# Kernel optimization log

Measured on AMD Instinct MI355X. Metric: run time of the kernel, lower is better.

The kernel has to match this reference:

```python
import jax, jax.numpy as jnp
import numpy as np

B, IN, H, U = 65536, 128, 256, 256

def lecun_tanh(x):
    return 1.7159 * jnp.tanh(0.666 * x)

def _xavier(key, shape):
    fan_out, fan_in = shape
    limit = np.sqrt(6.0 / (fan_in + fan_out))
    return jax.random.uniform(key, shape, jnp.float32, -limit, limit)

def setup_inputs() -> dict:
    key = jax.random.key(0)
    ks = jax.random.split(key, 12)
    return {
        "input": jax.random.normal(ks[0], (B, IN), jnp.float32),
        "hx": jax.random.normal(ks[1], (B, H), jnp.float32),
        "ts": jax.random.uniform(ks[2], (B, 1), jnp.float32),
        # backbone Linear(IN+H -> U)
        "Wb": _xavier(ks[3], (U, IN + H)),
        "bb": jnp.zeros((U,), jnp.float32),
        # ff1, ff2, time_a, time_b: Linear(U -> H)
        "W1": _xavier(ks[4], (H, U)),
        "b1": jnp.zeros((H,), jnp.float32),
        "W2": _xavier(ks[5], (H, U)),
        "b2": jnp.zeros((H,), jnp.float32),
        "Wa": _xavier(ks[6], (H, U)),
        "ba": jnp.zeros((H,), jnp.float32),
        "Wt": _xavier(ks[7], (H, U)),
        "bt": jnp.zeros((H,), jnp.float32),
    }

def reference(input, hx, ts, Wb, bb, W1, b1, W2, b2, Wa, ba, Wt, bt):
    # x = cat([input, hx]) -> backbone MLP (1 layer, LeCun tanh)
    x = jnp.concatenate([input, hx], axis=1)          # [B, IN+H]
    x = lecun_tanh(x @ Wb.T + bb)                     # [B, U]
    ff1 = jnp.tanh(x @ W1.T + b1)                     # [B, H]
    ff2 = jnp.tanh(x @ W2.T + b2)
    t_a = x @ Wa.T + ba
    t_b = x @ Wt.T + bt
    t_interp = jax.nn.sigmoid(t_a * ts + t_b)         # ts broadcasts [B,1]
    new_hidden = ff1 * (1.0 - t_interp) + t_interp * ff2
    return new_hidden
```

## Files before the change

kernel.cpp:

```cpp
#include <hip/hip_runtime.h>

typedef float v4f __attribute__((ext_vector_type(4)));
typedef short v8s __attribute__((ext_vector_type(8)));

#define BM 64

__device__ __forceinline__ unsigned short f2bf(float f) {
    union { float f; unsigned u; } v; v.f = f;
    unsigned u = v.u;
    u += 0x7FFFu + ((u >> 16) & 1u);
    return (unsigned short)(u >> 16);
}

__device__ __forceinline__ unsigned cvt_pk_bf16(float lo, float hi) {
    unsigned r;
    asm("v_cvt_pk_bf16_f32 %0, %1, %2" : "=v"(r) : "v"(lo), "v"(hi));
    return r;
}

#define LDS_BARRIER() do {                                        \
    asm volatile("s_waitcnt lgkmcnt(0)" ::: "memory");            \
    __builtin_amdgcn_s_barrier();                                 \
    __builtin_amdgcn_sched_barrier(0);                            \
} while (0)

#define SB() __builtin_amdgcn_sched_barrier(0)

__device__ __forceinline__ float fast_exp2(float x) {
#if __has_builtin(__builtin_amdgcn_exp2f)
    return __builtin_amdgcn_exp2f(x);
#else
    return exp2f(x);
#endif
}
__device__ __forceinline__ float fast_rcp(float x) {
#if __has_builtin(__builtin_amdgcn_rcpf)
    return __builtin_amdgcn_rcpf(x);
#else
    return 1.0f / x;
#endif
}
__device__ __forceinline__ float fast_tanh(float y) {
    float t = fast_exp2(y * 2.885390081777927f);
    return (t - 1.0f) * fast_rcp(t + 1.0f);
}
__device__ __forceinline__ float fast_sigmoid(float z) {
    float t = fast_exp2(-1.4426950408889634f * z);
    return fast_rcp(1.0f + t);
}

__global__ void prep_pack(const float* __restrict__ Wb, const float* __restrict__ W1,
                          const float* __restrict__ W2, const float* __restrict__ Wa,
                          const float* __restrict__ Wt, unsigned short* __restrict__ ws)
{
    int e = blockIdx.x * 256 + threadIdx.x;
    if (e >= 360448) return;
    const float* src; int K; int base;
    if (e < 98304)       { src = Wb; K = 384; base = 0; }
    else if (e < 163840) { src = W1; K = 256; base = 98304; }
    else if (e < 229376) { src = W2; K = 256; base = 163840; }
    else if (e < 294912) { src = Wa; K = 256; base = 229376; }
    else                 { src = Wt; K = 256; base = 294912; }
    int le   = e - base;
    int j    = le & 7;
    int lane = (le >> 3) & 63;
    int tile = le >> 9;
    int kt   = K >> 5;
    int ks   = tile % kt;
    int nt   = tile / kt;
    int n = nt * 16 + (lane & 15);
    int k = ks * 32 + (lane >> 4) * 8 + j;
    ws[e] = f2bf(src[n * K + k]);
}

__global__ __launch_bounds__(256, 2) void cfc_fused(
    const float* __restrict__ xin, const float* __restrict__ hx,
    const float* __restrict__ ts,
    const float* __restrict__ bb, const float* __restrict__ b1,
    const float* __restrict__ b2, const float* __restrict__ ba,
    const float* __restrict__ bt,
    const unsigned short* __restrict__ wpk,
    float* __restrict__ out)
{
    __shared__ unsigned short lds[16384];
    const int tid  = threadIdx.x;
    const int lane = tid & 63;
    const int w    = tid >> 6;
    const int row0 = blockIdx.x * BM;

    v8s br0[4], br1[4], br2[4];

#define BLOAD(S, DST) do {                                                    \
    _Pragma("unroll")                                                         \
    for (int i = 0; i < 4; ++i) {                                             \
        size_t goff;                                                          \
        if ((S) < 12) {                                                       \
            goff = (size_t)((w * 4 + i) * 12 + (S)) * 512;                    \
        } else {                                                              \
            int s2_ = (S) - 12, g_ = s2_ >> 3, ks_ = s2_ & 7;                 \
            goff = 98304u + (size_t)i * 65536                                 \
                 + (size_t)((w * 4 + g_) * 8 + ks_) * 512;                    \
        }                                                                     \
        DST[i] = *reinterpret_cast<const v8s*>(wpk + goff + (size_t)lane * 8);\
    }                                                                         \
} while (0)

#define ISSUE_IN(SRC, LD, BUF) do {                                           \
    _Pragma("unroll")                                                         \
    for (int it = 0; it < 4; ++it) {                                          \
        int i_ = tid + it * 256; int r_ = i_ >> 4; int c4_ = i_ & 15;         \
        BUF[it] = *(reinterpret_cast<const v4f*>((SRC) + (size_t)r_ * (LD)) + c4_); \
    }                                                                         \
} while (0)

#define WRITE_IN(BUF) do {                                                    \
    _Pragma("unroll")                                                         \
    for (int it = 0; it < 4; ++it) {                                          \
        int i_ = tid + it * 256; int r_ = i_ >> 4; int c4_ = i_ & 15;         \
        uint2 pk_;                                                            \
        pk_.x = cvt_pk_bf16(BUF[it][0], BUF[it][1]);                          \
        pk_.y = cvt_pk_bf16(BUF[it][2], BUF[it][3]);                          \
        int idx_ = (((r_ >> 4) * 2 + (c4_ >> 3)) * 64 + ((c4_ >> 1) & 3) * 16 \
                    + (r_ & 15)) * 8 + (c4_ & 1) * 4;                         \
        *reinterpret_cast<uint2*>(&lds[idx_]) = pk_;                          \
    }                                                                         \
} while (0)

#define P1STEP(S, CUR, PRE) do {                                              \
    BLOAD((S) + 2, PRE);                                                      \
    v8s aa_[4];                                                               \
    _Pragma("unroll")                                                         \
    for (int mt = 0; mt < 4; ++mt)                                            \
        aa_[mt] = *reinterpret_cast<const v8s*>(                              \
                      &lds[((mt * 2 + ((S) & 1)) * 64 + lane) * 8]);          \
    __builtin_amdgcn_s_setprio(1);                                            \
    _Pragma("unroll")                                                         \
    for (int nt = 0; nt < 4; ++nt)                                            \
        _Pragma("unroll")                                                     \
        for (int mt = 0; mt < 4; ++mt)                                        \
            acc[nt][mt] = __builtin_amdgcn_mfma_f32_16x16x32_bf16(            \
                              aa_[mt], CUR[nt], acc[nt][mt], 0, 0, 0);        \
    __builtin_amdgcn_s_setprio(0);                                            \
    SB();                                                                     \
} while (0)

#define P2STEP(S, KS, CUR, PRE) do {                                          \
    BLOAD((S) + 2, PRE);                                                      \
    v8s aa_[4];                                                               \
    _Pragma("unroll")                                                         \
    for (int mt = 0; mt < 4; ++mt)                                            \
        aa_[mt] = *reinterpret_cast<const v8s*>(                              \
                      &lds[((mt * 8 + (KS)) * 64 + lane) * 8]);               \
    __builtin_amdgcn_s_setprio(1);                                            \
    _Pragma("unroll")                                                         \
    for (int mat = 0; mat < 4; ++mat)                                         \
        _Pragma("unroll")                                                     \
        for (int mt = 0; mt < 4; ++mt)                                        \
            a2[mat][mt] = __builtin_amdgcn_mfma_f32_16x16x32_bf16(            \
                              aa_[mt], CUR[mat], a2[mat][mt], 0, 0, 0);       \
    __builtin_amdgcn_s_setprio(0);                                            \
    SB();                                                                     \
} while (0)

#define P2STEP_NS(S, KS, CUR) do {                                            \
    v8s aa_[4];                                                               \
    _Pragma("unroll")                                                         \
    for (int mt = 0; mt < 4; ++mt)                                            \
        aa_[mt] = *reinterpret_cast<const v8s*>(                              \
                      &lds[((mt * 8 + (KS)) * 64 + lane) * 8]);               \
    __builtin_amdgcn_s_setprio(1);                                            \
    _Pragma("unroll")                                                         \
    for (int mat = 0; mat < 4; ++mat)                                         \
        _Pragma("unroll")                                                     \
        for (int mt = 0; mt < 4; ++mt)                                        \
            a2[mat][mt] = __builtin_amdgcn_mfma_f32_16x16x32_bf16(            \
                              aa_[mt], CUR[mat], a2[mat][mt], 0, 0, 0);       \
    __builtin_amdgcn_s_setprio(0);                                            \
    SB();                                                                     \
} while (0)

#define GINIT(G) do {                                                         \
    const int n_ = w * 64 + (G) * 16 + (lane & 15);                           \
    float v1_ = b1[n_], v2_ = b2[n_], va_ = ba[n_], vt_ = bt[n_];             \
    v4f q1_ = {v1_,v1_,v1_,v1_}, q2_ = {v2_,v2_,v2_,v2_};                     \
    v4f qa_ = {va_,va_,va_,va_}, qt_ = {vt_,vt_,vt_,vt_};                     \
    _Pragma("unroll")                                                         \
    for (int mt = 0; mt < 4; ++mt) {                                          \
        a2[0][mt] = q1_; a2[1][mt] = q2_; a2[2][mt] = qa_; a2[3][mt] = qt_;   \
    }                                                                         \
} while (0)

#define EPI(G) do {                                                           \
    const int n_ = w * 64 + (G) * 16 + (lane & 15);                           \
    _Pragma("unroll")                                                         \
    for (int mt = 0; mt < 4; ++mt) {                                          \
        int rowb_ = row0 + mt * 16 + ((lane >> 4) << 2);                      \
        v4f tsv_ = *reinterpret_cast<const v4f*>(&ts[rowb_]);                 \
        _Pragma("unroll")                                                     \
        for (int r = 0; r < 4; ++r) {                                         \
            float ff1_ = fast_tanh(a2[0][mt][r]);                             \
            float ff2_ = fast_tanh(a2[1][mt][r]);                             \
            float ti_  = fast_sigmoid(a2[2][mt][r] * tsv_[r] + a2[3][mt][r]); \
            out[(size_t)(rowb_ + r) * 256 + n_] = ff1_ + ti_ * (ff2_ - ff1_); \
        }                                                                     \
    }                                                                         \
} while (0)

    v4f acc[4][4];
    #pragma unroll
    for (int nt = 0; nt < 4; ++nt) {
        float bv = bb[w * 64 + nt * 16 + (lane & 15)];
        v4f bvv = {bv, bv, bv, bv};
        #pragma unroll
        for (int mt = 0; mt < 4; ++mt) acc[nt][mt] = bvv;
    }

    v4f sA[4], sB[4];
    ISSUE_IN(xin + (size_t)row0 * 128, 128, sA);
    BLOAD(0, br0); BLOAD(1, br1);
    WRITE_IN(sA);
    ISSUE_IN(xin + (size_t)row0 * 128 + 64, 128, sB);
    LDS_BARRIER();
    P1STEP(0, br0, br2); P1STEP(1, br1, br0);
    LDS_BARRIER();
    WRITE_IN(sB);
    ISSUE_IN(hx + (size_t)row0 * 256, 256, sA);
    LDS_BARRIER();
    P1STEP(2, br2, br1); P1STEP(3, br0, br2);
    LDS_BARRIER();
    WRITE_IN(sA);
    ISSUE_IN(hx + (size_t)row0 * 256 + 64, 256, sB);
    LDS_BARRIER();
    P1STEP(4, br1, br0); P1STEP(5, br2, br1);
    LDS_BARRIER();
    WRITE_IN(sB);
    ISSUE_IN(hx + (size_t)row0 * 256 + 128, 256, sA);
    LDS_BARRIER();
    P1STEP(6, br0, br2); P1STEP(7, br1, br0);
    LDS_BARRIER();
    WRITE_IN(sA);
    ISSUE_IN(hx + (size_t)row0 * 256 + 192, 256, sB);
    LDS_BARRIER();
    P1STEP(8, br2, br1); P1STEP(9, br0, br2);
    LDS_BARRIER();
    WRITE_IN(sB);
    LDS_BARRIER();
    P1STEP(10, br1, br0); P1STEP(11, br2, br1);

    LDS_BARRIER();

    #pragma unroll
    for (int nt = 0; nt < 4; ++nt)
        #pragma unroll
        for (int mt = 0; mt < 4; ++mt)
            #pragma unroll
            for (int r = 0; r < 4; ++r) {
                float xv = 1.7159f * fast_tanh(0.666f * acc[nt][mt][r]);
                int idx = ((mt*8 + w*2 + (nt >> 1)) * 64
                           + ((nt & 1)*2 + ((lane >> 3) & 1)) * 16 + (lane >> 4)*4 + r) * 8
                          + (lane & 7);
                lds[idx] = f2bf(xv);
            }
    LDS_BARRIER();

    v4f a2[4][4];
    GINIT(0);
    P2STEP(12,0, br0, br2); P2STEP(13,1, br1, br0);
    P2STEP(14,2, br2, br1); P2STEP(15,3, br0, br2);
    P2STEP(16,4, br1, br0); P2STEP(17,5, br2, br1);
    P2STEP(18,6, br0, br2); P2STEP(19,7, br1, br0);
    EPI(0);
    GINIT(1);
    P2STEP(20,0, br2, br1); P2STEP(21,1, br0, br2);
    P2STEP(22,2, br1, br0); P2STEP(23,3, br2, br1);
    P2STEP(24,4, br0, br2); P2STEP(25,5, br1, br0);
    P2STEP(26,6, br2, br1); P2STEP(27,7, br0, br2);
    EPI(1);
    GINIT(2);
    P2STEP(28,0, br1, br0); P2STEP(29,1, br2, br1);
    P2STEP(30,2, br0, br2); P2STEP(31,3, br1, br0);
    P2STEP(32,4, br2, br1); P2STEP(33,5, br0, br2);
    P2STEP(34,6, br1, br0); P2STEP(35,7, br2, br1);
    EPI(2);
    GINIT(3);
    P2STEP(36,0, br0, br2); P2STEP(37,1, br1, br0);
    P2STEP(38,2, br2, br1); P2STEP(39,3, br0, br2);
    P2STEP(40,4, br1, br0); P2STEP(41,5, br2, br1);
    P2STEP_NS(42,6, br0);   P2STEP_NS(43,7, br1);
    EPI(3);

#undef BLOAD
#undef ISSUE_IN
#undef WRITE_IN
#undef P1STEP
#undef P2STEP
#undef P2STEP_NS
#undef GINIT
#undef EPI
}

extern "C" void kernel_launch(void* const* d_in, const int* in_sizes, int n_in,
                              void* d_out, int out_size, void* d_ws, size_t ws_size,
                              hipStream_t stream)
{
    const float* xin = (const float*)d_in[0];
    const float* hx  = (const float*)d_in[1];
    const float* ts  = (const float*)d_in[2];
    const float* Wb  = (const float*)d_in[3];
    const float* bb  = (const float*)d_in[4];
    const float* W1  = (const float*)d_in[5];
    const float* b1  = (const float*)d_in[6];
    const float* W2  = (const float*)d_in[7];
    const float* b2  = (const float*)d_in[8];
    const float* Wa  = (const float*)d_in[9];
    const float* ba  = (const float*)d_in[10];
    const float* Wt  = (const float*)d_in[11];
    const float* bt  = (const float*)d_in[12];

    if (ws_size < 360448 * sizeof(unsigned short)) return;
    unsigned short* wpk = (unsigned short*)d_ws;

    prep_pack<<<1408, 256, 0, stream>>>(Wb, W1, W2, Wa, Wt, wpk);
    cfc_fused<<<1024, 256, 0, stream>>>(xin, hx, ts, bb, b1, b2, ba, bt, wpk,
                                        (float*)d_out);
}
```

Baseline: 68.40 us.

## Split fused CfC kernel into backbone and head kernels via bf16 workspace

Splits the single fused kernel into two launches when the workspace is large enough. The first computes the backbone layer and writes the activated x as bf16 in MFMA fragment layout to global memory. The second reads those fragments straight from global memory (no LDS) to run the four head GEMMs and the epilogue, and uses higher occupancy (launch bounds 3). It also collapses the fused kernel's double input staging buffer into one. The aim is to relieve register and LDS pressure in each phase, at the cost of an extra 32 MB round trip through global memory and one more launch.

```diff
diff --git a/kernel.cpp b/kernel.cpp
--- a/kernel.cpp
+++ b/kernel.cpp
@@ -73,6 +73,243 @@
     ws[e] = f2bf(src[n * K + k]);
 }
 
+__global__ __launch_bounds__(256, 2) void cfc_p1(
+    const float* __restrict__ xin, const float* __restrict__ hx,
+    const float* __restrict__ bb, const unsigned short* __restrict__ wpk,
+    unsigned short* __restrict__ Xg)
+{
+    __shared__ unsigned short lds[16384];
+    const int tid  = threadIdx.x;
+    const int lane = tid & 63;
+    const int w    = tid >> 6;
+    const int row0 = blockIdx.x * BM;
+
+    v8s br0[4], br1[4], br2[4];
+
+#define BLOADA(S, DST) do {                                                   \
+    _Pragma("unroll")                                                         \
+    for (int i = 0; i < 4; ++i) {                                             \
+        size_t goff = (size_t)((w * 4 + i) * 12 + ((S) % 12)) * 512;          \
+        DST[i] = *reinterpret_cast<const v8s*>(wpk + goff + (size_t)lane * 8);\
+    }                                                                         \
+} while (0)
+
+#define ISSUE_INA(SRC, LD, BUF) do {                                          \
+    _Pragma("unroll")                                                         \
+    for (int it = 0; it < 4; ++it) {                                          \
+        int i_ = tid + it * 256; int r_ = i_ >> 4; int c4_ = i_ & 15;         \
+        BUF[it] = *(reinterpret_cast<const v4f*>((SRC) + (size_t)r_ * (LD)) + c4_); \
+    }                                                                         \
+} while (0)
+
+#define WRITE_INA(BUF) do {                                                   \
+    _Pragma("unroll")                                                         \
+    for (int it = 0; it < 4; ++it) {                                          \
+        int i_ = tid + it * 256; int r_ = i_ >> 4; int c4_ = i_ & 15;         \
+        uint2 pk_;                                                            \
+        pk_.x = cvt_pk_bf16(BUF[it][0], BUF[it][1]);                          \
+        pk_.y = cvt_pk_bf16(BUF[it][2], BUF[it][3]);                          \
+        int idx_ = (((r_ >> 4) * 2 + (c4_ >> 3)) * 64 + ((c4_ >> 1) & 3) * 16 \
+                    + (r_ & 15)) * 8 + (c4_ & 1) * 4;                         \
+        *reinterpret_cast<uint2*>(&lds[idx_]) = pk_;                          \
+    }                                                                         \
+} while (0)
+
+#define P1STEPA(S, CUR, PRE) do {                                             \
+    BLOADA((S) + 2, PRE);                                                     \
+    v8s aa_[4];                                                               \
+    _Pragma("unroll")                                                         \
+    for (int mt = 0; mt < 4; ++mt)                                            \
+        aa_[mt] = *reinterpret_cast<const v8s*>(                              \
+                      &lds[((mt * 2 + ((S) & 1)) * 64 + lane) * 8]);          \
+    __builtin_amdgcn_s_setprio(1);                                            \
+    _Pragma("unroll")                                                         \
+    for (int nt = 0; nt < 4; ++nt)                                            \
+        _Pragma("unroll")                                                     \
+        for (int mt = 0; mt < 4; ++mt)                                        \
+            acc[nt][mt] = __builtin_amdgcn_mfma_f32_16x16x32_bf16(            \
+                              aa_[mt], CUR[nt], acc[nt][mt], 0, 0, 0);        \
+    __builtin_amdgcn_s_setprio(0);                                            \
+    SB();                                                                     \
+} while (0)
+
+    v4f acc[4][4];
+    #pragma unroll
+    for (int nt = 0; nt < 4; ++nt) {
+        float bv = bb[w * 64 + nt * 16 + (lane & 15)];
+        v4f bvv = {bv, bv, bv, bv};
+        #pragma unroll
+        for (int mt = 0; mt < 4; ++mt) acc[nt][mt] = bvv;
+    }
+
+    v4f sA[4];
+    ISSUE_INA(xin + (size_t)row0 * 128, 128, sA);
+    BLOADA(0, br0); BLOADA(1, br1);
+    WRITE_INA(sA);
+    ISSUE_INA(xin + (size_t)row0 * 128 + 64, 128, sA);
+    LDS_BARRIER();
+    P1STEPA(0, br0, br2); P1STEPA(1, br1, br0);
+    LDS_BARRIER();
+    WRITE_INA(sA);
+    ISSUE_INA(hx + (size_t)row0 * 256, 256, sA);
+    LDS_BARRIER();
+    P1STEPA(2, br2, br1); P1STEPA(3, br0, br2);
+    LDS_BARRIER();
+    WRITE_INA(sA);
+    ISSUE_INA(hx + (size_t)row0 * 256 + 64, 256, sA);
+    LDS_BARRIER();
+    P1STEPA(4, br1, br0); P1STEPA(5, br2, br1);
+    LDS_BARRIER();
+    WRITE_INA(sA);
+    ISSUE_INA(hx + (size_t)row0 * 256 + 128, 256, sA);
+    LDS_BARRIER();
+    P1STEPA(6, br0, br2); P1STEPA(7, br1, br0);
+    LDS_BARRIER();
+    WRITE_INA(sA);
+    ISSUE_INA(hx + (size_t)row0 * 256 + 192, 256, sA);
+    LDS_BARRIER();
+    P1STEPA(8, br2, br1); P1STEPA(9, br0, br2);
+    LDS_BARRIER();
+    WRITE_INA(sA);
+    LDS_BARRIER();
+    P1STEPA(10, br1, br0); P1STEPA(11, br2, br1);
+
+    LDS_BARRIER();
+
+    #pragma unroll
+    for (int nt = 0; nt < 4; ++nt)
+        #pragma unroll
+        for (int mt = 0; mt < 4; ++mt)
+            #pragma unroll
+            for (int r = 0; r < 4; ++r) {
+                float xv = 1.7159f * fast_tanh(0.666f * acc[nt][mt][r]);
+                int idx = ((mt*8 + w*2 + (nt >> 1)) * 64
+                           + ((nt & 1)*2 + ((lane >> 3) & 1)) * 16 + (lane >> 4)*4 + r) * 8
+                          + (lane & 7);
+                lds[idx] = f2bf(xv);
+            }
+    LDS_BARRIER();
+
+    unsigned short* xb = Xg + (size_t)blockIdx.x * 16384;
+    #pragma unroll
+    for (int it = 0; it < 8; ++it) {
+        int i = tid + it * 256;
+        *reinterpret_cast<v8s*>(xb + (size_t)i * 8) =
+            *reinterpret_cast<const v8s*>(&lds[i * 8]);
+    }
+#undef BLOADA
+#undef ISSUE_INA
+#undef WRITE_INA
+#undef P1STEPA
+}
+
+__global__ __launch_bounds__(256, 3) void cfc_p2(
+    const float* __restrict__ ts,
+    const float* __restrict__ b1, const float* __restrict__ b2,
+    const float* __restrict__ ba, const float* __restrict__ bt,
+    const unsigned short* __restrict__ wpk,
+    const unsigned short* __restrict__ Xg, float* __restrict__ out)
+{
+    const int tid  = threadIdx.x;
+    const int lane = tid & 63;
+    const int w    = tid >> 6;
+    const int row0 = blockIdx.x * BM;
+    const unsigned short* Xb = Xg + (size_t)blockIdx.x * 16384;
+
+    v8s br0[4], br1[4];
+
+#define BLOADB(S, DST) do {                                                   \
+    _Pragma("unroll")                                                         \
+    for (int i = 0; i < 4; ++i) {                                             \
+        size_t goff = 98304u + (size_t)i * 65536                              \
+                    + (size_t)(w * 32 + (S)) * 512;                           \
+        DST[i] = *reinterpret_cast<const v8s*>(wpk + goff + (size_t)lane * 8);\
+    }                                                                         \
+} while (0)
+
+#define P2BODYB(KS, CUR) do {                                                 \
+    v8s aa_[4];                                                               \
+    _Pragma("unroll")                                                         \
+    for (int mt = 0; mt < 4; ++mt)                                            \
+        aa_[mt] = *reinterpret_cast<const v8s*>(                              \
+                      Xb + (size_t)(((mt * 8 + (KS)) * 64 + lane)) * 8);      \
+    __builtin_amdgcn_s_setprio(1);                                            \
+    _Pragma("unroll")                                                         \
+    for (int mat = 0; mat < 4; ++mat)                                         \
+        _Pragma("unroll")                                                     \
+        for (int mt = 0; mt < 4; ++mt)                                        \
+            a2[mat][mt] = __builtin_amdgcn_mfma_f32_16x16x32_bf16(            \
+                              aa_[mt], CUR[mat], a2[mat][mt], 0, 0, 0);       \
+    __builtin_amdgcn_s_setprio(0);                                            \
+    SB();                                                                     \
+} while (0)
+
+#define P2SB(S, KS, CUR, PRE) do { BLOADB((S) + 1, PRE); P2BODYB(KS, CUR); } while (0)
+#define P2SB_NS(S, KS, CUR)   do { P2BODYB(KS, CUR); } while (0)
+
+#define GINITB(G) do {                                                        \
+    const int n_ = w * 64 + (G) * 16 + (lane & 15);                           \
+    float v1_ = b1[n_], v2_ = b2[n_], va_ = ba[n_], vt_ = bt[n_];             \
+    v4f q1_ = {v1_,v1_,v1_,v1_}, q2_ = {v2_,v2_,v2_,v2_};                     \
+    v4f qa_ = {va_,va_,va_,va_}, qt_ = {vt_,vt_,vt_,vt_};                     \
+    _Pragma("unroll")                                                         \
+    for (int mt = 0; mt < 4; ++mt) {                                          \
+        a2[0][mt] = q1_; a2[1][mt] = q2_; a2[2][mt] = qa_; a2[3][mt] = qt_;   \
+    }                                                                         \
+} while (0)
+
+#define EPIB(G) do {                                                          \
+    const int n_ = w * 64 + (G) * 16 + (lane & 15);                           \
+    _Pragma("unroll")                                                         \
+    for (int mt = 0; mt < 4; ++mt) {                                          \
+        int rowb_ = row0 + mt * 16 + ((lane >> 4) << 2);                      \
+        v4f tsv_ = *reinterpret_cast<const v4f*>(&ts[rowb_]);                 \
+        _Pragma("unroll")                                                     \
+        for (int r = 0; r < 4; ++r) {                                         \
+            float ff1_ = fast_tanh(a2[0][mt][r]);                             \
+            float ff2_ = fast_tanh(a2[1][mt][r]);                             \
+            float ti_  = fast_sigmoid(a2[2][mt][r] * tsv_[r] + a2[3][mt][r]); \
+            out[(size_t)(rowb_ + r) * 256 + n_] = ff1_ + ti_ * (ff2_ - ff1_); \
+        }                                                                     \
+    }                                                                         \
+} while (0)
+
+    v4f a2[4][4];
+    BLOADB(0, br0);
+
+    GINITB(0);
+    P2SB(0,0, br0, br1);  P2SB(1,1, br1, br0);
+    P2SB(2,2, br0, br1);  P2SB(3,3, br1, br0);
+    P2SB(4,4, br0, br1);  P2SB(5,5, br1, br0);
+    P2SB(6,6, br0, br1);  P2SB(7,7, br1, br0);
+    EPIB(0);
+    GINITB(1);
+    P2SB(8,0, br0, br1);  P2SB(9,1, br1, br0);
+    P2SB(10,2, br0, br1); P2SB(11,3, br1, br0);
+    P2SB(12,4, br0, br1); P2SB(13,5, br1, br0);
+    P2SB(14,6, br0, br1); P2SB(15,7, br1, br0);
+    EPIB(1);
+    GINITB(2);
+    P2SB(16,0, br0, br1); P2SB(17,1, br1, br0);
+    P2SB(18,2, br0, br1); P2SB(19,3, br1, br0);
+    P2SB(20,4, br0, br1); P2SB(21,5, br1, br0);
+    P2SB(22,6, br0, br1); P2SB(23,7, br1, br0);
+    EPIB(2);
+    GINITB(3);
+    P2SB(24,0, br0, br1); P2SB(25,1, br1, br0);
+    P2SB(26,2, br0, br1); P2SB(27,3, br1, br0);
+    P2SB(28,4, br0, br1); P2SB(29,5, br1, br0);
+    P2SB(30,6, br0, br1); P2SB_NS(31,7, br1);
+    EPIB(3);
+
+#undef BLOADB
+#undef P2BODYB
+#undef P2SB
+#undef P2SB_NS
+#undef GINITB
+#undef EPIB
+}
+
 __global__ __launch_bounds__(256, 2) void cfc_fused(
     const float* __restrict__ xin, const float* __restrict__ hx,
     const float* __restrict__ ts,
@@ -215,35 +452,35 @@
         for (int mt = 0; mt < 4; ++mt) acc[nt][mt] = bvv;
     }
 
-    v4f sA[4], sB[4];
+    v4f sA[4];
     ISSUE_IN(xin + (size_t)row0 * 128, 128, sA);
     BLOAD(0, br0); BLOAD(1, br1);
     WRITE_IN(sA);
-    ISSUE_IN(xin + (size_t)row0 * 128 + 64, 128, sB);
+    ISSUE_IN(xin + (size_t)row0 * 128 + 64, 128, sA);
     LDS_BARRIER();
     P1STEP(0, br0, br2); P1STEP(1, br1, br0);
     LDS_BARRIER();
-    WRITE_IN(sB);
+    WRITE_IN(sA);
     ISSUE_IN(hx + (size_t)row0 * 256, 256, sA);
     LDS_BARRIER();
     P1STEP(2, br2, br1); P1STEP(3, br0, br2);
     LDS_BARRIER();
     WRITE_IN(sA);
-    ISSUE_IN(hx + (size_t)row0 * 256 + 64, 256, sB);
+    ISSUE_IN(hx + (size_t)row0 * 256 + 64, 256, sA);
     LDS_BARRIER();
     P1STEP(4, br1, br0); P1STEP(5, br2, br1);
     LDS_BARRIER();
-    WRITE_IN(sB);
+    WRITE_IN(sA);
     ISSUE_IN(hx + (size_t)row0 * 256 + 128, 256, sA);
     LDS_BARRIER();
     P1STEP(6, br0, br2); P1STEP(7, br1, br0);
     LDS_BARRIER();
     WRITE_IN(sA);
-    ISSUE_IN(hx + (size_t)row0 * 256 + 192, 256, sB);
+    ISSUE_IN(hx + (size_t)row0 * 256 + 192, 256, sA);
     LDS_BARRIER();
     P1STEP(8, br2, br1); P1STEP(9, br0, br2);
     LDS_BARRIER();
-    WRITE_IN(sB);
+    WRITE_IN(sA);
     LDS_BARRIER();
     P1STEP(10, br1, br0); P1STEP(11, br2, br1);
 
@@ -317,10 +554,20 @@
     const float* Wt  = (const float*)d_in[11];
     const float* bt  = (const float*)d_in[12];
 
-    if (ws_size < 360448 * sizeof(unsigned short)) return;
+    const size_t wpk_bytes = 360448ull * 2;
+    const size_t xg_bytes  = 65536ull * 256 * 2;
+    if (ws_size < wpk_bytes) return;
+
     unsigned short* wpk = (unsigned short*)d_ws;
-
     prep_pack<<<1408, 256, 0, stream>>>(Wb, W1, W2, Wa, Wt, wpk);
-    cfc_fused<<<1024, 256, 0, stream>>>(xin, hx, ts, bb, b1, b2, ba, bt, wpk,
-                                        (float*)d_out);
-}
+
+    if (ws_size >= wpk_bytes + xg_bytes) {
+        unsigned short* Xg = wpk + 360448;
+        cfc_p1<<<1024, 256, 0, stream>>>(xin, hx, bb, wpk, Xg);
+        cfc_p2<<<1024, 256, 0, stream>>>(ts, b1, b2, ba, bt, wpk, Xg,
+                                         (float*)d_out);
+    } else {
+        cfc_fused<<<1024, 256, 0, stream>>>(xin, hx, ts, bb, b1, b2, ba, bt,
+                                            wpk, (float*)d_out);
+    }
+}
```

Result: slower. 123.7 us (+80.8%).
